# Kernel tuning notes

Hardware: AMD Instinct MI355X
Metric: run time of the kernel (lower is better)

Reference implementation:

```python
import jax, jax.numpy as jnp
import numpy as np

N = 50000      # nodes
E = 800000     # edges (avg degree 16)
F_IN = 128     # input feature dim
HID = 128      # 2 * out_classes
OUT = 64       # out_classes


def setup_inputs() -> dict:
    key = jax.random.key(0)
    ks = jax.random.split(key, 12)
    x = jax.random.normal(ks[0], (N, F_IN), jnp.float32)
    edge_index = jax.random.randint(ks[1], (2, E), 0, N, jnp.int32)
    def lin(k, fi, fo):
        return jax.random.normal(k, (fi, fo), jnp.float32) / np.float32(np.sqrt(fi))
    return {
        "x": x,
        "edge_index": edge_index,
        "W1": lin(ks[2], F_IN, HID), "b1": jnp.zeros((HID,), jnp.float32),
        "W2": lin(ks[3], HID, HID),  "b2": jnp.zeros((HID,), jnp.float32),
        "W3": lin(ks[4], HID, HID),  "b3": jnp.zeros((HID,), jnp.float32),
        "jk_w": jax.random.normal(ks[5], (3,), jnp.float32),
        "fc_W": lin(ks[6], HID, OUT), "fc_b": jnp.zeros((OUT,), jnp.float32),
    }


def _gcn_conv(h, W, b, row, col, n):
    """PyG GCNConv: linear -> add self-loops -> sym-normalized aggregate -> bias."""
    h = h @ W                                        # [n, d_out]
    loops = jnp.arange(n, dtype=row.dtype)
    r = jnp.concatenate([row, loops])                # sources
    c = jnp.concatenate([col, loops])                # targets
    deg = jax.ops.segment_sum(jnp.ones_like(c, h.dtype), c, num_segments=n)
    dinv = jnp.where(deg > 0, jax.lax.rsqrt(deg), 0.0)
    norm = dinv[r] * dinv[c]                         # [E+n]
    msg = h[r] * norm[:, None]                       # gather + scale
    return jax.ops.segment_sum(msg, c, num_segments=n) + b


def _neighbor_mean(h, row, col, n):
    """sample_neighbors with scale_factor=2: exact mean over out-neighbors,
    own feature when degree == 0 (top-k branch is provably dead code)."""
    s = jax.ops.segment_sum(h[col], row, num_segments=n)
    deg = jax.ops.segment_sum(jnp.ones_like(row, h.dtype), row, num_segments=n)
    mean = s / jnp.maximum(deg, 1.0)[:, None]
    return jnp.where((deg > 0)[:, None], mean, h)


def reference(x, edge_index, W1, b1, W2, b2, W3, b3, jk_w, fc_W, fc_b):
    row, col = edge_index[0], edge_index[1]
    n = x.shape[0]
    # layer 0: GCN -> ReLU -> (dropout: eval identity) -> neighbor sampling
    h0 = jax.nn.relu(_gcn_conv(x, W1, b1, row, col, n))
    h0 = _neighbor_mean(h0, row, col, n)
    # layer 1: GCN -> ReLU; historical-activation update is identity on first call
    h1 = jax.nn.relu(_gcn_conv(h0, W2, b2, row, col, n))
    # layer 2
    h2 = jax.nn.relu(_gcn_conv(h1, W3, b3, row, col, n))
    # dynamic JK aggregation
    w = jax.nn.softmax(jk_w)
    h = w[0] * h0 + w[1] * h1 + w[2] * h2
    return h @ fc_W + fc_b
```

## Files before the change

### kernel.cpp

```cpp
#include <hip/hip_runtime.h>
#include <stdint.h>

typedef unsigned int  uint32;
typedef unsigned short u16;

typedef short bfx8 __attribute__((ext_vector_type(8)));
typedef float f32x4 __attribute__((ext_vector_type(4)));
typedef float f32x2 __attribute__((ext_vector_type(2)));
typedef uint32 u32x4 __attribute__((ext_vector_type(4)));

#define NBP 256
#define CH  2048
#define BS  4608

__device__ __forceinline__ float b2f(u16 u) {
    union { uint32 i; float f; } v; v.i = ((uint32)u) << 16; return v.f;
}
__device__ __forceinline__ u16 f2b(float f) {
    union { float f; uint32 i; } v; v.f = f;
    uint32 u = v.i;
    return (u16)((u + 0x7fffu + ((u >> 16) & 1u)) >> 16);
}
__device__ __forceinline__ float blo(uint32 u) {
    union { uint32 i; float f; } v; v.i = u << 16; return v.f;
}
__device__ __forceinline__ float bhi(uint32 u) {
    union { uint32 i; float f; } v; v.i = u & 0xffff0000u; return v.f;
}
__device__ __forceinline__ uint32 packbf(float a, float b) {
    return (uint32)f2b(a) | ((uint32)f2b(b) << 16);
}
__device__ __forceinline__ void splitf(float x, u16& h, u16& l) {
    h = f2b(x);
    l = f2b(x - b2f(h));
}
__device__ __forceinline__ void acc4(float* s, u32x4 v) {
    s[0] += blo(v.x); s[1] += bhi(v.x);
    s[2] += blo(v.y); s[3] += bhi(v.y);
    s[4] += blo(v.z); s[5] += bhi(v.z);
    s[6] += blo(v.w); s[7] += bhi(v.w);
}

__global__ __launch_bounds__(256) void k_init(
    int* __restrict__ curC, int* __restrict__ curR,
    const float* __restrict__ W1, const float* __restrict__ W2,
    const float* __restrict__ W3, const float* __restrict__ fcW,
    u16* __restrict__ WTh, u16* __restrict__ WTl, int WTN) {
    int t = threadIdx.x;
    if (blockIdx.x == 0) {
        curC[t] = t * BS;
        curR[t] = t * BS;
        return;
    }
    int i = ((int)blockIdx.x - 1) * 256 + t;
    if (i >= WTN) return;
    float w;
    if (i < 3 * 16384) {
        int m = i >> 14, j = i & 16383;
        int fo = j >> 7, fi = j & 127;
        const float* W = (m == 0) ? W1 : (m == 1) ? W2 : W3;
        w = W[fi * 128 + fo];
    } else {
        int j = i - 3 * 16384;
        int fo = j >> 7, fi = j & 127;
        w = fcW[fi * 64 + fo];
    }
    u16 h, l; splitf(w, h, l);
    WTh[i] = h; WTl[i] = l;
}

__global__ __launch_bounds__(256) void k_partC(
    const int* __restrict__ row, const int* __restrict__ col, int E,
    int* __restrict__ curC, int* __restrict__ curR,
    uint32* __restrict__ partC, uint32* __restrict__ partR) {
    __shared__ uint32 stagedC[CH], stagedR[CH];
    __shared__ int hp[NBP], expk[NBP], curp[NBP], runC[NBP], runR[NBP];
    __shared__ int wsum[4];
    int t = threadIdx.x;
    int lane = t & 63, wid = t >> 6;
    int base = blockIdx.x * CH;
    int n = E - base; if (n > CH) n = CH;

    int er[8], ec[8];
#pragma unroll
    for (int j = 0; j < 8; ++j) {
        int i = t + j * 256;
        if (i < n) { er[j] = row[base + i]; ec[j] = col[base + i]; }
        else er[j] = -1;
    }
    hp[t] = 0;
    __syncthreads();
#pragma unroll
    for (int j = 0; j < 8; ++j) {
        if (er[j] >= 0) {
            atomicAdd(&hp[ec[j] >> 8], 1);
            atomicAdd(&hp[er[j] >> 8], 0x10000);
        }
    }
    __syncthreads();
    int v = hp[t];
    int x = v;
#pragma unroll
    for (int d = 1; d < 64; d <<= 1) {
        int u = __shfl_up(x, d);
        if (lane >= d) x += u;
    }
    if (lane == 63) wsum[wid] = x;
    __syncthreads();
    int add = 0;
    for (int i = 0; i < wid; ++i) add += wsum[i];
    int ex = x + add - v;
    expk[t] = ex;
    curp[t] = ex;
    int vC = v & 0xffff, vR = v >> 16;
    runC[t] = vC ? atomicAdd(&curC[t], vC) : 0;
    runR[t] = vR ? atomicAdd(&curR[t], vR) : 0;
    __syncthreads();
#pragma unroll
    for (int j = 0; j < 8; ++j) {
        if (er[j] >= 0) {
            int cb = ec[j] >> 8, rb = er[j] >> 8;
            int pC = atomicAdd(&curp[cb], 1) & 0xffff;
            stagedC[pC] = ((uint32)ec[j] << 16) | (uint32)er[j];
            int pR = atomicAdd(&curp[rb], 0x10000) >> 16;
            stagedR[pR] = ((uint32)er[j] << 16) | (uint32)ec[j];
        }
    }
    __syncthreads();
    for (int i = t; i < n; i += 256) {
        uint32 pv = stagedC[i];
        int b = pv >> 24;
        partC[runC[b] + (i - (expk[b] & 0xffff))] = pv;
    }
    for (int i = t; i < n; i += 256) {
        uint32 pv = stagedR[i];
        int b = pv >> 24;
        partR[runR[b] + (i - (expk[b] >> 16))] = pv;
    }
}

__global__ __launch_bounds__(256) void k_fillD(
    const uint32* __restrict__ partC, const uint32* __restrict__ partR,
    const int* __restrict__ curC, const int* __restrict__ curR,
    int* __restrict__ off_in, int* __restrict__ end_in,
    int* __restrict__ off_out, int* __restrict__ end_out,
    u16* __restrict__ csr_src, u16* __restrict__ csr_dst,
    float* __restrict__ dinv, int NB, int N) {
    int part = ((int)blockIdx.x >= NB) ? 1 : 0;
    int b = (int)blockIdx.x - part * NB;
    const uint32* arr = part ? partR : partC;
    const int* curA   = part ? curR : curC;
    int* offA         = part ? off_out : off_in;
    int* endA         = part ? end_out : end_in;
    u16* csr          = part ? csr_dst : csr_src;
    int t = threadIdx.x;
    int lane = t & 63, wid = t >> 6;
    int base = b * BS, end = curA[b];
    __shared__ int cnt[NBP], cur[NBP];
    __shared__ int wsum[4];
    cnt[t] = 0;
    __syncthreads();
    for (int i = base + t; i < end; i += 256)
        atomicAdd(&cnt[(arr[i] >> 16) & 255], 1);
    __syncthreads();
    int v = cnt[t];
    int x = v;
#pragma unroll
    for (int d = 1; d < 64; d <<= 1) {
        int u = __shfl_up(x, d);
        if (lane >= d) x += u;
    }
    if (lane == 63) wsum[wid] = x;
    __syncthreads();
    int add = 0;
    for (int i = 0; i < wid; ++i) add += wsum[i];
    int ex = x + add - v;
    cur[t] = ex;
    int node = (b << 8) + t;
    if (node < N) {
        offA[node] = base + ex;
        endA[node] = base + ex + v;
        if (part == 0) dinv[node] = rsqrtf((float)(v + 1));
    }
    __syncthreads();
    for (int i = base + t; i < end; i += 256) {
        uint32 pv = arr[i];
        int local = (pv >> 16) & 255;
        int pos = atomicAdd(&cur[local], 1);
        csr[base + pos] = (u16)(pv & 0xffffu);
    }
}

__global__ __launch_bounds__(256) void k_gemm0(
    const float* __restrict__ A, const u16* __restrict__ WTh, const u16* __restrict__ WTl,
    const float* __restrict__ dinv, u16* __restrict__ G, int M) {
    const int lane = threadIdx.x & 63;
    const int q = lane >> 4, l = lane & 15;
    int rbase = blockIdx.x * 128 + (threadIdx.x >> 6) * 32;
    if (rbase >= M) return;
    int r0 = rbase + l;      if (r0 >= M) r0 = M - 1;
    int r1 = rbase + 16 + l; if (r1 >= M) r1 = M - 1;

    f32x4 acc[2][8];
#pragma unroll
    for (int i = 0; i < 2; ++i)
#pragma unroll
        for (int j = 0; j < 8; ++j) acc[i][j] = (f32x4){0.f, 0.f, 0.f, 0.f};

#pragma unroll
    for (int kc = 0; kc < 4; ++kc) {
        int k0 = kc * 32 + q * 8;
        bfx8 ah0, ah1;
        {
            f32x4 a = *(const f32x4*)(A + (size_t)r0 * 128 + k0);
            f32x4 b = *(const f32x4*)(A + (size_t)r0 * 128 + k0 + 4);
            float xx[8] = {a[0], a[1], a[2], a[3], b[0], b[1], b[2], b[3]};
#pragma unroll
            for (int j = 0; j < 8; ++j) ah0[j] = (short)f2b(xx[j]);
        }
        {
            f32x4 a = *(const f32x4*)(A + (size_t)r1 * 128 + k0);
            f32x4 b = *(const f32x4*)(A + (size_t)r1 * 128 + k0 + 4);
            float xx[8] = {a[0], a[1], a[2], a[3], b[0], b[1], b[2], b[3]};
#pragma unroll
            for (int j = 0; j < 8; ++j) ah1[j] = (short)f2b(xx[j]);
        }
#pragma unroll
        for (int ct = 0; ct < 8; ++ct) {
            bfx8 bh = *(const bfx8*)(WTh + (ct * 16 + l) * 128 + k0);
            bfx8 bl = *(const bfx8*)(WTl + (ct * 16 + l) * 128 + k0);
            acc[0][ct] = __builtin_amdgcn_mfma_f32_16x16x32_bf16(ah0, bh, acc[0][ct], 0, 0, 0);
            acc[0][ct] = __builtin_amdgcn_mfma_f32_16x16x32_bf16(ah0, bl, acc[0][ct], 0, 0, 0);
            acc[1][ct] = __builtin_amdgcn_mfma_f32_16x16x32_bf16(ah1, bh, acc[1][ct], 0, 0, 0);
            acc[1][ct] = __builtin_amdgcn_mfma_f32_16x16x32_bf16(ah1, bl, acc[1][ct], 0, 0, 0);
        }
    }
#pragma unroll
    for (int rs = 0; rs < 2; ++rs) {
#pragma unroll
        for (int rr = 0; rr < 4; ++rr) {
            int rw = rbase + rs * 16 + q * 4 + rr;
            if (rw < M) {
                float dv = dinv[rw];
#pragma unroll
                for (int ct = 0; ct < 8; ++ct)
                    G[(size_t)rw * 128 + ct * 16 + l] = f2b(acc[rs][ct][rr] * dv);
            }
        }
    }
}

__global__ __launch_bounds__(256) void k_gemm1p(
    const u16* __restrict__ Ah,
    const u16* __restrict__ WTh, const u16* __restrict__ WTl,
    const float* __restrict__ dinv, u16* __restrict__ G, int M) {
    const int lane = threadIdx.x & 63;
    const int q = lane >> 4, l = lane & 15;
    int rbase = blockIdx.x * 128 + (threadIdx.x >> 6) * 32;
    if (rbase >= M) return;
    int r0 = rbase + l;      if (r0 >= M) r0 = M - 1;
    int r1 = rbase + 16 + l; if (r1 >= M) r1 = M - 1;

    f32x4 acc[2][8];
#pragma unroll
    for (int i = 0; i < 2; ++i)
#pragma unroll
        for (int j = 0; j < 8; ++j) acc[i][j] = (f32x4){0.f, 0.f, 0.f, 0.f};

#pragma unroll
    for (int kc = 0; kc < 4; ++kc) {
        int k0 = kc * 32 + q * 8;
        bfx8 ah0 = *(const bfx8*)(Ah + (size_t)r0 * 128 + k0);
        bfx8 ah1 = *(const bfx8*)(Ah + (size_t)r1 * 128 + k0);
#pragma unroll
        for (int ct = 0; ct < 8; ++ct) {
            bfx8 bh = *(const bfx8*)(WTh + (ct * 16 + l) * 128 + k0);
            bfx8 bl = *(const bfx8*)(WTl + (ct * 16 + l) * 128 + k0);
            acc[0][ct] = __builtin_amdgcn_mfma_f32_16x16x32_bf16(ah0, bh, acc[0][ct], 0, 0, 0);
            acc[0][ct] = __builtin_amdgcn_mfma_f32_16x16x32_bf16(ah0, bl, acc[0][ct], 0, 0, 0);
            acc[1][ct] = __builtin_amdgcn_mfma_f32_16x16x32_bf16(ah1, bh, acc[1][ct], 0, 0, 0);
            acc[1][ct] = __builtin_amdgcn_mfma_f32_16x16x32_bf16(ah1, bl, acc[1][ct], 0, 0, 0);
        }
    }
#pragma unroll
    for (int rs = 0; rs < 2; ++rs) {
#pragma unroll
        for (int rr = 0; rr < 4; ++rr) {
            int rw = rbase + rs * 16 + q * 4 + rr;
            if (rw < M) {
                float dv = dinv[rw];
#pragma unroll
                for (int ct = 0; ct < 8; ++ct)
                    G[(size_t)rw * 128 + ct * 16 + l] = f2b(acc[rs][ct][rr] * dv);
            }
        }
    }
}

__global__ __launch_bounds__(256) void k_agg(
    const u32x4* __restrict__ g4, const u16* __restrict__ csr,
    const int* __restrict__ off, const int* __restrict__ endo,
    const float* __restrict__ dinv,
    const float* __restrict__ bias, u32x4* __restrict__ outH4, int n) {
    int w = (blockIdx.x * 256 + threadIdx.x) >> 6;
    if (w >= n) return;
    int lane = threadIdx.x & 63;
    int gq = lane >> 4, c = lane & 15;
    float s[8];
#pragma unroll
    for (int k = 0; k < 8; ++k) s[k] = 0.f;
    int e = off[w], e1 = endo[w];
    for (; e + 32 <= e1; e += 32) {
        int ix[8];
#pragma unroll
        for (int j = 0; j < 8; ++j) ix[j] = __builtin_nontemporal_load(csr + e + j * 4 + gq);
        u32x4 vv[8];
#pragma unroll
        for (int j = 0; j < 8; ++j) vv[j] = g4[(size_t)ix[j] * 16 + c];
#pragma unroll
        for (int j = 0; j < 8; ++j) acc4(s, vv[j]);
    }
    for (; e + 16 <= e1; e += 16) {
        int ix[4];
#pragma unroll
        for (int j = 0; j < 4; ++j) ix[j] = __builtin_nontemporal_load(csr + e + j * 4 + gq);
        u32x4 vv[4];
#pragma unroll
        for (int j = 0; j < 4; ++j) vv[j] = g4[(size_t)ix[j] * 16 + c];
#pragma unroll
        for (int j = 0; j < 4; ++j) acc4(s, vv[j]);
    }
    for (; e < e1; e += 4) {
        int idx = e + gq;
        if (idx < e1) {
            int ii = __builtin_nontemporal_load(csr + idx);
            acc4(s, g4[(size_t)ii * 16 + c]);
        }
    }
#pragma unroll
    for (int k = 0; k < 8; ++k) {
        s[k] += __shfl_xor(s[k], 16);
        s[k] += __shfl_xor(s[k], 32);
    }
    if (lane < 16) {
        u32x4 sv = g4[(size_t)w * 16 + lane];
        acc4(s, sv);
        float dc = dinv[w];
        const f32x4* B4 = (const f32x4*)bias;
        f32x4 ba = B4[lane * 2], bb = B4[lane * 2 + 1];
        float o[8];
#pragma unroll
        for (int k = 0; k < 4; ++k) o[k] = fmaxf(fmaf(s[k], dc, ba[k]), 0.f);
#pragma unroll
        for (int k = 0; k < 4; ++k) o[4 + k] = fmaxf(fmaf(s[4 + k], dc, bb[k]), 0.f);
        u32x4 ov;
        ov.x = packbf(o[0], o[1]); ov.y = packbf(o[2], o[3]);
        ov.z = packbf(o[4], o[5]); ov.w = packbf(o[6], o[7]);
        __builtin_nontemporal_store(ov, &outH4[(size_t)w * 16 + lane]);
    }
}

__global__ __launch_bounds__(256) void k_mean(
    const u32x4* __restrict__ h4, const u16* __restrict__ csr,
    const int* __restrict__ off, const int* __restrict__ endo,
    u32x4* __restrict__ outH4, int n) {
    int w = (blockIdx.x * 256 + threadIdx.x) >> 6;
    if (w >= n) return;
    int lane = threadIdx.x & 63;
    int gq = lane >> 4, c = lane & 15;
    float s[8];
#pragma unroll
    for (int k = 0; k < 8; ++k) s[k] = 0.f;
    int e = off[w], e1 = endo[w];
    int d = e1 - e;
    for (; e + 32 <= e1; e += 32) {
        int ix[8];
#pragma unroll
        for (int j = 0; j < 8; ++j) ix[j] = __builtin_nontemporal_load(csr + e + j * 4 + gq);
        u32x4 vv[8];
#pragma unroll
        for (int j = 0; j < 8; ++j) vv[j] = h4[(size_t)ix[j] * 16 + c];
#pragma unroll
        for (int j = 0; j < 8; ++j) acc4(s, vv[j]);
    }
    for (; e + 16 <= e1; e += 16) {
        int ix[4];
#pragma unroll
        for (int j = 0; j < 4; ++j) ix[j] = __builtin_nontemporal_load(csr + e + j * 4 + gq);
        u32x4 vv[4];
#pragma unroll
        for (int j = 0; j < 4; ++j) vv[j] = h4[(size_t)ix[j] * 16 + c];
#pragma unroll
        for (int j = 0; j < 4; ++j) acc4(s, vv[j]);
    }
    for (; e < e1; e += 4) {
        int idx = e + gq;
        if (idx < e1) {
            int ii = __builtin_nontemporal_load(csr + idx);
            acc4(s, h4[(size_t)ii * 16 + c]);
        }
    }
#pragma unroll
    for (int k = 0; k < 8; ++k) {
        s[k] += __shfl_xor(s[k], 16);
        s[k] += __shfl_xor(s[k], 32);
    }
    if (lane < 16) {
        u32x4 ov;
        if (d > 0) {
            float inv = 1.f / (float)d;
            ov.x = packbf(s[0] * inv, s[1] * inv);
            ov.y = packbf(s[2] * inv, s[3] * inv);
            ov.z = packbf(s[4] * inv, s[5] * inv);
            ov.w = packbf(s[6] * inv, s[7] * inv);
        } else {
            ov = h4[(size_t)w * 16 + lane];
        }
        __builtin_nontemporal_store(ov, &outH4[(size_t)w * 16 + lane]);
    }
}

__global__ __launch_bounds__(256) void k_final(
    const u16* __restrict__ h0, const u16* __restrict__ h1,
    const u16* __restrict__ h2, const float* __restrict__ jkw,
    const u16* __restrict__ fcWTh, const u16* __restrict__ fcWTl,
    const float* __restrict__ fcb, float* __restrict__ out, int M) {
    float a0 = jkw[0], a1 = jkw[1], a2 = jkw[2];
    float mx = fmaxf(a0, fmaxf(a1, a2));
    float e0 = expf(a0 - mx), e1 = expf(a1 - mx), e2 = expf(a2 - mx);
    float inv = 1.f / (e0 + e1 + e2);
    float w0 = e0 * inv, w1 = e1 * inv, w2 = e2 * inv;

    const int lane = threadIdx.x & 63;
    const int q = lane >> 4, l = lane & 15;
    int rbase = blockIdx.x * 128 + (threadIdx.x >> 6) * 32;
    if (rbase >= M) return;
    int r0 = rbase + l;      if (r0 >= M) r0 = M - 1;
    int r1 = rbase + 16 + l; if (r1 >= M) r1 = M - 1;

    f32x4 acc[2][4];
#pragma unroll
    for (int i = 0; i < 2; ++i)
#pragma unroll
        for (int j = 0; j < 4; ++j) acc[i][j] = (f32x4){0.f, 0.f, 0.f, 0.f};

    union U8 { bfx8 v; u16 u[8]; };

#pragma unroll
    for (int kc = 0; kc < 4; ++kc) {
        int k0 = kc * 32 + q * 8;
        bfx8 ah[2];
        const int rr2[2] = {r0, r1};
#pragma unroll
        for (int half = 0; half < 2; ++half) {
            size_t o = (size_t)rr2[half] * 128 + k0;
            U8 x0, x1, x2, rh;
            x0.v = *(const bfx8*)(h0 + o);
            x1.v = *(const bfx8*)(h1 + o);
            x2.v = *(const bfx8*)(h2 + o);
#pragma unroll
            for (int j = 0; j < 8; ++j) {
                float c = w0 * b2f(x0.u[j]) + w1 * b2f(x1.u[j]) + w2 * b2f(x2.u[j]);
                rh.u[j] = f2b(c);
            }
            ah[half] = rh.v;
        }
#pragma unroll
        for (int ct = 0; ct < 4; ++ct) {
            bfx8 bh = *(const bfx8*)(fcWTh + (ct * 16 + l) * 128 + k0);
            bfx8 bl = *(const bfx8*)(fcWTl + (ct * 16 + l) * 128 + k0);
#pragma unroll
            for (int half = 0; half < 2; ++half) {
                acc[half][ct] = __builtin_amdgcn_mfma_f32_16x16x32_bf16(ah[half], bh, acc[half][ct], 0, 0, 0);
                acc[half][ct] = __builtin_amdgcn_mfma_f32_16x16x32_bf16(ah[half], bl, acc[half][ct], 0, 0, 0);
            }
        }
    }
#pragma unroll
    for (int rs = 0; rs < 2; ++rs) {
#pragma unroll
        for (int rr = 0; rr < 4; ++rr) {
            int rw = rbase + rs * 16 + q * 4 + rr;
            if (rw < M) {
#pragma unroll
                for (int ct = 0; ct < 4; ++ct) {
                    int cc = ct * 16 + l;
                    out[(size_t)rw * 64 + cc] = acc[rs][ct][rr] + fcb[cc];
                }
            }
        }
    }
}

extern "C" void kernel_launch(void* const* d_in, const int* in_sizes, int n_in,
                              void* d_out, int out_size, void* d_ws, size_t ws_size,
                              hipStream_t stream) {
    const int N = in_sizes[0] / 128;
    const int E = in_sizes[1] / 2;
    const int NB = (N + 255) >> 8;

    const float* x    = (const float*)d_in[0];
    const int* row    = (const int*)d_in[1];
    const int* col    = row + E;
    const float* W1   = (const float*)d_in[2];
    const float* b1   = (const float*)d_in[3];
    const float* W2   = (const float*)d_in[4];
    const float* b2   = (const float*)d_in[5];
    const float* W3   = (const float*)d_in[6];
    const float* b3   = (const float*)d_in[7];
    const float* jkw  = (const float*)d_in[8];
    const float* fcW  = (const float*)d_in[9];
    const float* fcb  = (const float*)d_in[10];
    float* outp       = (float*)d_out;

    char* ws = (char*)d_ws;
    size_t off = 0;
    auto alloc = [&](size_t bytes) -> char* {
        char* p = ws + off;
        off += (bytes + 255) & ~(size_t)255;
        return p;
    };
    int* curC   = (int*)alloc((size_t)NBP * sizeof(int));
    int* curR   = (int*)alloc((size_t)NBP * sizeof(int));
    int* off_in  = (int*)alloc((size_t)N * sizeof(int));
    int* end_in  = (int*)alloc((size_t)N * sizeof(int));
    int* off_out = (int*)alloc((size_t)N * sizeof(int));
    int* end_out = (int*)alloc((size_t)N * sizeof(int));
    uint32* partC = (uint32*)alloc((size_t)NBP * BS * sizeof(uint32));
    uint32* partR = (uint32*)alloc((size_t)NBP * BS * sizeof(uint32));
    u16* csr_src = (u16*)alloc((size_t)NBP * BS * sizeof(u16));
    u16* csr_dst = (u16*)alloc((size_t)NBP * BS * sizeof(u16));
    float* dinv  = (float*)alloc((size_t)N * sizeof(float));
    const int WTN = 3 * 16384 + 8192;
    u16* WTh = (u16*)alloc((size_t)WTN * sizeof(u16));
    u16* WTl = (u16*)alloc((size_t)WTN * sizeof(u16));
    size_t FB = (size_t)N * 128 * sizeof(u16);
    u16* gbuf = (u16*)alloc(FB);
    u16* t0   = (u16*)alloc(FB);
    u16* h0   = (u16*)alloc(FB);
    u16* h1   = (u16*)alloc(FB);
    u16* h2   = (u16*)alloc(FB);

    const int B = 256;
    int Gh = (E + CH - 1) / CH;
    int Gg = (N + 127) / 128;
    int Gwt = (WTN + B - 1) / B;

    k_init<<<1 + Gwt, B, 0, stream>>>(curC, curR, W1, W2, W3, fcW, WTh, WTl, WTN);
    k_partC<<<Gh, B, 0, stream>>>(row, col, E, curC, curR, partC, partR);
    k_fillD<<<2 * NB, B, 0, stream>>>(partC, partR, curC, curR,
                                      off_in, end_in, off_out, end_out,
                                      csr_src, csr_dst, dinv, NB, N);
    k_gemm0<<<Gg, B, 0, stream>>>(x, WTh, WTl, dinv, gbuf, N);

    int aggG = (N + 3) / 4;

    k_agg<<<aggG, B, 0, stream>>>((const u32x4*)gbuf, csr_src, off_in, end_in, dinv,
                                  b1, (u32x4*)t0, N);
    k_mean<<<aggG, B, 0, stream>>>((const u32x4*)t0, csr_dst, off_out, end_out,
                                   (u32x4*)h0, N);
    k_gemm1p<<<Gg, B, 0, stream>>>(h0, WTh + 16384, WTl + 16384, dinv, gbuf, N);
    k_agg<<<aggG, B, 0, stream>>>((const u32x4*)gbuf, csr_src, off_in, end_in, dinv,
                                  b2, (u32x4*)h1, N);
    k_gemm1p<<<Gg, B, 0, stream>>>(h1, WTh + 2 * 16384, WTl + 2 * 16384, dinv, gbuf, N);
    k_agg<<<aggG, B, 0, stream>>>((const u32x4*)gbuf, csr_src, off_in, end_in, dinv,
                                  b3, (u32x4*)h2, N);
    k_final<<<Gg, B, 0, stream>>>(h0, h1, h2, jkw,
                                  WTh + 3 * 16384, WTl + 3 * 16384, fcb, outp, N);
}
```

Baseline: 345.3 us.

## Merge CSR fill with first GEMM and apply source dinv inside aggregation

The CSR fill kernel and the layer-0 GEMM now share one launch. Extra blocks run the x@W1 GEMM without dinv scaling, so they no longer depend on the degree computation and can overlap the fill work. A new k_agg0 applies the per-source dinv scale during the gather instead, which adds a dinv load per edge. The change also drops the 32-edge unrolled loop and the nontemporal loads and stores from the aggregation and mean kernels. That lowers register pressure but reduces memory-level parallelism.

Measured after the change: 327.3 us. 5.2% less time.

```diff
diff --git a/kernel.cpp b/kernel.cpp
--- a/kernel.cpp
+++ b/kernel.cpp
@@ -6,7 +6,6 @@
 
 typedef short bfx8 __attribute__((ext_vector_type(8)));
 typedef float f32x4 __attribute__((ext_vector_type(4)));
-typedef float f32x2 __attribute__((ext_vector_type(2)));
 typedef uint32 u32x4 __attribute__((ext_vector_type(4)));
 
 #define NBP 256
@@ -39,6 +38,12 @@
     s[2] += blo(v.y); s[3] += bhi(v.y);
     s[4] += blo(v.z); s[5] += bhi(v.z);
     s[6] += blo(v.w); s[7] += bhi(v.w);
+}
+__device__ __forceinline__ void acc4f(float* s, u32x4 v, float d) {
+    s[0] = fmaf(blo(v.x), d, s[0]); s[1] = fmaf(bhi(v.x), d, s[1]);
+    s[2] = fmaf(blo(v.y), d, s[2]); s[3] = fmaf(bhi(v.y), d, s[3]);
+    s[4] = fmaf(blo(v.z), d, s[4]); s[5] = fmaf(bhi(v.z), d, s[5]);
+    s[6] = fmaf(blo(v.w), d, s[6]); s[7] = fmaf(bhi(v.w), d, s[7]);
 }
 
 __global__ __launch_bounds__(256) void k_init(
@@ -139,112 +144,116 @@
     }
 }
 
-__global__ __launch_bounds__(256) void k_fillD(
+__global__ __launch_bounds__(256) void k_fillDg0(
     const uint32* __restrict__ partC, const uint32* __restrict__ partR,
     const int* __restrict__ curC, const int* __restrict__ curR,
     int* __restrict__ off_in, int* __restrict__ end_in,
     int* __restrict__ off_out, int* __restrict__ end_out,
     u16* __restrict__ csr_src, u16* __restrict__ csr_dst,
-    float* __restrict__ dinv, int NB, int N) {
-    int part = ((int)blockIdx.x >= NB) ? 1 : 0;
-    int b = (int)blockIdx.x - part * NB;
-    const uint32* arr = part ? partR : partC;
-    const int* curA   = part ? curR : curC;
-    int* offA         = part ? off_out : off_in;
-    int* endA         = part ? end_out : end_in;
-    u16* csr          = part ? csr_dst : csr_src;
-    int t = threadIdx.x;
-    int lane = t & 63, wid = t >> 6;
-    int base = b * BS, end = curA[b];
+    float* __restrict__ dinv, int NB, int N,
+    const float* __restrict__ A, const u16* __restrict__ WTh,
+    const u16* __restrict__ WTl, u16* __restrict__ G) {
     __shared__ int cnt[NBP], cur[NBP];
     __shared__ int wsum[4];
-    cnt[t] = 0;
-    __syncthreads();
-    for (int i = base + t; i < end; i += 256)
-        atomicAdd(&cnt[(arr[i] >> 16) & 255], 1);
-    __syncthreads();
-    int v = cnt[t];
-    int x = v;
-#pragma unroll
-    for (int d = 1; d < 64; d <<= 1) {
-        int u = __shfl_up(x, d);
-        if (lane >= d) x += u;
-    }
-    if (lane == 63) wsum[wid] = x;
-    __syncthreads();
-    int add = 0;
-    for (int i = 0; i < wid; ++i) add += wsum[i];
-    int ex = x + add - v;
-    cur[t] = ex;
-    int node = (b << 8) + t;
-    if (node < N) {
-        offA[node] = base + ex;
-        endA[node] = base + ex + v;
-        if (part == 0) dinv[node] = rsqrtf((float)(v + 1));
-    }
-    __syncthreads();
-    for (int i = base + t; i < end; i += 256) {
-        uint32 pv = arr[i];
-        int local = (pv >> 16) & 255;
-        int pos = atomicAdd(&cur[local], 1);
-        csr[base + pos] = (u16)(pv & 0xffffu);
-    }
-}
-
-__global__ __launch_bounds__(256) void k_gemm0(
-    const float* __restrict__ A, const u16* __restrict__ WTh, const u16* __restrict__ WTl,
-    const float* __restrict__ dinv, u16* __restrict__ G, int M) {
-    const int lane = threadIdx.x & 63;
-    const int q = lane >> 4, l = lane & 15;
-    int rbase = blockIdx.x * 128 + (threadIdx.x >> 6) * 32;
-    if (rbase >= M) return;
-    int r0 = rbase + l;      if (r0 >= M) r0 = M - 1;
-    int r1 = rbase + 16 + l; if (r1 >= M) r1 = M - 1;
-
-    f32x4 acc[2][8];
-#pragma unroll
-    for (int i = 0; i < 2; ++i)
-#pragma unroll
-        for (int j = 0; j < 8; ++j) acc[i][j] = (f32x4){0.f, 0.f, 0.f, 0.f};
-
-#pragma unroll
-    for (int kc = 0; kc < 4; ++kc) {
-        int k0 = kc * 32 + q * 8;
-        bfx8 ah0, ah1;
-        {
-            f32x4 a = *(const f32x4*)(A + (size_t)r0 * 128 + k0);
-            f32x4 b = *(const f32x4*)(A + (size_t)r0 * 128 + k0 + 4);
-            float xx[8] = {a[0], a[1], a[2], a[3], b[0], b[1], b[2], b[3]};
-#pragma unroll
-            for (int j = 0; j < 8; ++j) ah0[j] = (short)f2b(xx[j]);
-        }
-        {
-            f32x4 a = *(const f32x4*)(A + (size_t)r1 * 128 + k0);
-            f32x4 b = *(const f32x4*)(A + (size_t)r1 * 128 + k0 + 4);
-            float xx[8] = {a[0], a[1], a[2], a[3], b[0], b[1], b[2], b[3]};
-#pragma unroll
-            for (int j = 0; j < 8; ++j) ah1[j] = (short)f2b(xx[j]);
-        }
-#pragma unroll
-        for (int ct = 0; ct < 8; ++ct) {
-            bfx8 bh = *(const bfx8*)(WTh + (ct * 16 + l) * 128 + k0);
-            bfx8 bl = *(const bfx8*)(WTl + (ct * 16 + l) * 128 + k0);
-            acc[0][ct] = __builtin_amdgcn_mfma_f32_16x16x32_bf16(ah0, bh, acc[0][ct], 0, 0, 0);
-            acc[0][ct] = __builtin_amdgcn_mfma_f32_16x16x32_bf16(ah0, bl, acc[0][ct], 0, 0, 0);
-            acc[1][ct] = __builtin_amdgcn_mfma_f32_16x16x32_bf16(ah1, bh, acc[1][ct], 0, 0, 0);
-            acc[1][ct] = __builtin_amdgcn_mfma_f32_16x16x32_bf16(ah1, bl, acc[1][ct], 0, 0, 0);
-        }
-    }
-#pragma unroll
-    for (int rs = 0; rs < 2; ++rs) {
-#pragma unroll
-        for (int rr = 0; rr < 4; ++rr) {
-            int rw = rbase + rs * 16 + q * 4 + rr;
-            if (rw < M) {
-                float dv = dinv[rw];
-#pragma unroll
-                for (int ct = 0; ct < 8; ++ct)
-                    G[(size_t)rw * 128 + ct * 16 + l] = f2b(acc[rs][ct][rr] * dv);
+    int t = threadIdx.x;
+
+    if ((int)blockIdx.x < 2 * NB) {
+        int part = ((int)blockIdx.x >= NB) ? 1 : 0;
+        int b = (int)blockIdx.x - part * NB;
+        const uint32* arr = part ? partR : partC;
+        const int* curA   = part ? curR : curC;
+        int* offA         = part ? off_out : off_in;
+        int* endA         = part ? end_out : end_in;
+        u16* csr          = part ? csr_dst : csr_src;
+        int lane = t & 63, wid = t >> 6;
+        int base = b * BS, end = curA[b];
+        cnt[t] = 0;
+        __syncthreads();
+        for (int i = base + t; i < end; i += 256)
+            atomicAdd(&cnt[(arr[i] >> 16) & 255], 1);
+        __syncthreads();
+        int v = cnt[t];
+        int x = v;
+#pragma unroll
+        for (int d = 1; d < 64; d <<= 1) {
+            int u = __shfl_up(x, d);
+            if (lane >= d) x += u;
+        }
+        if (lane == 63) wsum[wid] = x;
+        __syncthreads();
+        int add = 0;
+        for (int i = 0; i < wid; ++i) add += wsum[i];
+        int ex = x + add - v;
+        cur[t] = ex;
+        int node = (b << 8) + t;
+        if (node < N) {
+            offA[node] = base + ex;
+            endA[node] = base + ex + v;
+            if (part == 0) dinv[node] = rsqrtf((float)(v + 1));
+        }
+        __syncthreads();
+        for (int i = base + t; i < end; i += 256) {
+            uint32 pv = arr[i];
+            int local = (pv >> 16) & 255;
+            int pos = atomicAdd(&cur[local], 1);
+            csr[base + pos] = (u16)(pv & 0xffffu);
+        }
+        return;
+    }
+
+    {
+        int gb = (int)blockIdx.x - 2 * NB;
+        const int lane = t & 63;
+        const int q = lane >> 4, l = lane & 15;
+        int rbase = gb * 128 + (t >> 6) * 32;
+        if (rbase >= N) return;
+        int r0 = rbase + l;      if (r0 >= N) r0 = N - 1;
+        int r1 = rbase + 16 + l; if (r1 >= N) r1 = N - 1;
+
+        f32x4 acc[2][8];
+#pragma unroll
+        for (int i = 0; i < 2; ++i)
+#pragma unroll
+            for (int j = 0; j < 8; ++j) acc[i][j] = (f32x4){0.f, 0.f, 0.f, 0.f};
+
+#pragma unroll
+        for (int kc = 0; kc < 4; ++kc) {
+            int k0 = kc * 32 + q * 8;
+            bfx8 ah0, ah1;
+            {
+                f32x4 a = *(const f32x4*)(A + (size_t)r0 * 128 + k0);
+                f32x4 b = *(const f32x4*)(A + (size_t)r0 * 128 + k0 + 4);
+                float xx[8] = {a[0], a[1], a[2], a[3], b[0], b[1], b[2], b[3]};
+#pragma unroll
+                for (int j = 0; j < 8; ++j) ah0[j] = (short)f2b(xx[j]);
+            }
+            {
+                f32x4 a = *(const f32x4*)(A + (size_t)r1 * 128 + k0);
+                f32x4 b = *(const f32x4*)(A + (size_t)r1 * 128 + k0 + 4);
+                float xx[8] = {a[0], a[1], a[2], a[3], b[0], b[1], b[2], b[3]};
+#pragma unroll
+                for (int j = 0; j < 8; ++j) ah1[j] = (short)f2b(xx[j]);
+            }
+#pragma unroll
+            for (int ct = 0; ct < 8; ++ct) {
+                bfx8 bh = *(const bfx8*)(WTh + (ct * 16 + l) * 128 + k0);
+                bfx8 bl = *(const bfx8*)(WTl + (ct * 16 + l) * 128 + k0);
+                acc[0][ct] = __builtin_amdgcn_mfma_f32_16x16x32_bf16(ah0, bh, acc[0][ct], 0, 0, 0);
+                acc[0][ct] = __builtin_amdgcn_mfma_f32_16x16x32_bf16(ah0, bl, acc[0][ct], 0, 0, 0);
+                acc[1][ct] = __builtin_amdgcn_mfma_f32_16x16x32_bf16(ah1, bh, acc[1][ct], 0, 0, 0);
+                acc[1][ct] = __builtin_amdgcn_mfma_f32_16x16x32_bf16(ah1, bl, acc[1][ct], 0, 0, 0);
+            }
+        }
+#pragma unroll
+        for (int rs = 0; rs < 2; ++rs) {
+#pragma unroll
+            for (int rr = 0; rr < 4; ++rr) {
+                int rw = rbase + rs * 16 + q * 4 + rr;
+                if (rw < N) {
+#pragma unroll
+                    for (int ct = 0; ct < 8; ++ct)
+                        G[(size_t)rw * 128 + ct * 16 + l] = f2b(acc[rs][ct][rr]);
+                }
             }
         }
     }
@@ -297,6 +306,60 @@
     }
 }
 
+__global__ __launch_bounds__(256) void k_agg0(
+    const u32x4* __restrict__ g4, const u16* __restrict__ csr,
+    const int* __restrict__ off, const int* __restrict__ endo,
+    const float* __restrict__ dinv,
+    const float* __restrict__ bias, u32x4* __restrict__ outH4, int n) {
+    int w = (blockIdx.x * 256 + threadIdx.x) >> 6;
+    if (w >= n) return;
+    int lane = threadIdx.x & 63;
+    int gq = lane >> 4, c = lane & 15;
+    float s[8];
+#pragma unroll
+    for (int k = 0; k < 8; ++k) s[k] = 0.f;
+    int e = off[w], e1 = endo[w];
+    for (; e + 16 <= e1; e += 16) {
+        int ix[4];
+#pragma unroll
+        for (int j = 0; j < 4; ++j) ix[j] = csr[e + j * 4 + gq];
+        u32x4 vv[4];
+        float dd[4];
+#pragma unroll
+        for (int j = 0; j < 4; ++j) { vv[j] = g4[(size_t)ix[j] * 16 + c]; dd[j] = dinv[ix[j]]; }
+#pragma unroll
+        for (int j = 0; j < 4; ++j) acc4f(s, vv[j], dd[j]);
+    }
+    for (; e < e1; e += 4) {
+        int idx = e + gq;
+        if (idx < e1) {
+            int ii = csr[idx];
+            acc4f(s, g4[(size_t)ii * 16 + c], dinv[ii]);
+        }
+    }
+#pragma unroll
+    for (int k = 0; k < 8; ++k) {
+        s[k] += __shfl_xor(s[k], 16);
+        s[k] += __shfl_xor(s[k], 32);
+    }
+    if (lane < 16) {
+        float dc = dinv[w];
+        u32x4 sv = g4[(size_t)w * 16 + lane];
+        acc4f(s, sv, dc);
+        const f32x4* B4 = (const f32x4*)bias;
+        f32x4 ba = B4[lane * 2], bb = B4[lane * 2 + 1];
+        float o[8];
+#pragma unroll
+        for (int k = 0; k < 4; ++k) o[k] = fmaxf(fmaf(s[k], dc, ba[k]), 0.f);
+#pragma unroll
+        for (int k = 0; k < 4; ++k) o[4 + k] = fmaxf(fmaf(s[4 + k], dc, bb[k]), 0.f);
+        u32x4 ov;
+        ov.x = packbf(o[0], o[1]); ov.y = packbf(o[2], o[3]);
+        ov.z = packbf(o[4], o[5]); ov.w = packbf(o[6], o[7]);
+        outH4[(size_t)w * 16 + lane] = ov;
+    }
+}
+
 __global__ __launch_bounds__(256) void k_agg(
     const u32x4* __restrict__ g4, const u16* __restrict__ csr,
     const int* __restrict__ off, const int* __restrict__ endo,
@@ -310,20 +373,10 @@
 #pragma unroll
     for (int k = 0; k < 8; ++k) s[k] = 0.f;
     int e = off[w], e1 = endo[w];
-    for (; e + 32 <= e1; e += 32) {
-        int ix[8];
-#pragma unroll
-        for (int j = 0; j < 8; ++j) ix[j] = __builtin_nontemporal_load(csr + e + j * 4 + gq);
-        u32x4 vv[8];
-#pragma unroll
-        for (int j = 0; j < 8; ++j) vv[j] = g4[(size_t)ix[j] * 16 + c];
-#pragma unroll
-        for (int j = 0; j < 8; ++j) acc4(s, vv[j]);
-    }
     for (; e + 16 <= e1; e += 16) {
         int ix[4];
 #pragma unroll
-        for (int j = 0; j < 4; ++j) ix[j] = __builtin_nontemporal_load(csr + e + j * 4 + gq);
+        for (int j = 0; j < 4; ++j) ix[j] = csr[e + j * 4 + gq];
         u32x4 vv[4];
 #pragma unroll
         for (int j = 0; j < 4; ++j) vv[j] = g4[(size_t)ix[j] * 16 + c];
@@ -333,7 +386,7 @@
     for (; e < e1; e += 4) {
         int idx = e + gq;
         if (idx < e1) {
-            int ii = __builtin_nontemporal_load(csr + idx);
+            int ii = csr[idx];
             acc4(s, g4[(size_t)ii * 16 + c]);
         }
     }
@@ -356,7 +409,7 @@
         u32x4 ov;
         ov.x = packbf(o[0], o[1]); ov.y = packbf(o[2], o[3]);
         ov.z = packbf(o[4], o[5]); ov.w = packbf(o[6], o[7]);
-        __builtin_nontemporal_store(ov, &outH4[(size_t)w * 16 + lane]);
+        outH4[(size_t)w * 16 + lane] = ov;
     }
 }
 
@@ -373,20 +426,10 @@
     for (int k = 0; k < 8; ++k) s[k] = 0.f;
     int e = off[w], e1 = endo[w];
     int d = e1 - e;
-    for (; e + 32 <= e1; e += 32) {
-        int ix[8];
-#pragma unroll
-        for (int j = 0; j < 8; ++j) ix[j] = __builtin_nontemporal_load(csr + e + j * 4 + gq);
-        u32x4 vv[8];
-#pragma unroll
-        for (int j = 0; j < 8; ++j) vv[j] = h4[(size_t)ix[j] * 16 + c];
-#pragma unroll
-        for (int j = 0; j < 8; ++j) acc4(s, vv[j]);
-    }
     for (; e + 16 <= e1; e += 16) {
         int ix[4];
 #pragma unroll
-        for (int j = 0; j < 4; ++j) ix[j] = __builtin_nontemporal_load(csr + e + j * 4 + gq);
+        for (int j = 0; j < 4; ++j) ix[j] = csr[e + j * 4 + gq];
         u32x4 vv[4];
 #pragma unroll
         for (int j = 0; j < 4; ++j) vv[j] = h4[(size_t)ix[j] * 16 + c];
@@ -396,7 +439,7 @@
     for (; e < e1; e += 4) {
         int idx = e + gq;
         if (idx < e1) {
-            int ii = __builtin_nontemporal_load(csr + idx);
+            int ii = csr[idx];
             acc4(s, h4[(size_t)ii * 16 + c]);
         }
     }
@@ -416,7 +459,7 @@
         } else {
             ov = h4[(size_t)w * 16 + lane];
         }
-        __builtin_nontemporal_store(ov, &outH4[(size_t)w * 16 + lane]);
+        outH4[(size_t)w * 16 + lane] = ov;
     }
 }
 
@@ -548,15 +591,15 @@
 
     k_init<<<1 + Gwt, B, 0, stream>>>(curC, curR, W1, W2, W3, fcW, WTh, WTl, WTN);
     k_partC<<<Gh, B, 0, stream>>>(row, col, E, curC, curR, partC, partR);
-    k_fillD<<<2 * NB, B, 0, stream>>>(partC, partR, curC, curR,
-                                      off_in, end_in, off_out, end_out,
-                                      csr_src, csr_dst, dinv, NB, N);
-    k_gemm0<<<Gg, B, 0, stream>>>(x, WTh, WTl, dinv, gbuf, N);
+    k_fillDg0<<<2 * NB + Gg, B, 0, stream>>>(partC, partR, curC, curR,
+                                             off_in, end_in, off_out, end_out,
+                                             csr_src, csr_dst, dinv, NB, N,
+                                             x, WTh, WTl, gbuf);
 
     int aggG = (N + 3) / 4;
 
-    k_agg<<<aggG, B, 0, stream>>>((const u32x4*)gbuf, csr_src, off_in, end_in, dinv,
-                                  b1, (u32x4*)t0, N);
+    k_agg0<<<aggG, B, 0, stream>>>((const u32x4*)gbuf, csr_src, off_in, end_in, dinv,
+                                   b1, (u32x4*)t0, N);
     k_mean<<<aggG, B, 0, stream>>>((const u32x4*)t0, csr_dst, off_out, end_out,
                                    (u32x4*)h0, N);
     k_gemm1p<<<Gg, B, 0, stream>>>(h0, WTh + 16384, WTl + 16384, dinv, gbuf, N);
```
